# Performance work log

Hardware: AMD Instinct MI355X
Metric: run time of the kernel (lower is better)

## Reference

```python
import jax, jax.numpy as jnp
import numpy as np

EMBED_DIM = 1024
NUM_HEADS = 16
HEAD_DIM = EMBED_DIM // NUM_HEADS


def setup_inputs() -> dict:
    key = jax.random.key(0)
    k1, k2, k3, k4, k5 = jax.random.split(key, 5)
    B, T, C = 2, 2048, EMBED_DIM
    x = jax.random.normal(k1, (B, T, C), dtype=jnp.float32)
    # Linear params stored as (in, out) so y = x @ W + b
    s = 1.0 / np.sqrt(C)
    W_qkv = jax.random.uniform(k2, (C, 3 * C), minval=-s, maxval=s, dtype=jnp.float32)
    b_qkv = jax.random.uniform(k3, (3 * C,), minval=-s, maxval=s, dtype=jnp.float32)
    W_out = jax.random.uniform(k4, (C, C), minval=-s, maxval=s, dtype=jnp.float32)
    b_out = jax.random.uniform(k5, (C,), minval=-s, maxval=s, dtype=jnp.float32)
    return {"x": x, "W_qkv": W_qkv, "b_qkv": b_qkv, "W_out": W_out, "b_out": b_out}


def reference(x, W_qkv, b_qkv, W_out, b_out):
    B, T, C = x.shape
    H, D = NUM_HEADS, HEAD_DIM
    qkv = x @ W_qkv + b_qkv                       # [B, T, 3C]
    qkv = qkv.reshape(B, T, 3, H, D)
    q = qkv[:, :, 0].transpose(0, 2, 1, 3)        # [B, H, T, D]
    k = qkv[:, :, 1].transpose(0, 2, 1, 3)
    v = qkv[:, :, 2].transpose(0, 2, 1, 3)
    scores = jnp.einsum('bhqd,bhkd->bhqk', q, k) / jnp.sqrt(jnp.float32(D))
    causal = jnp.tril(jnp.ones((T, T), dtype=bool))
    scores = jnp.where(causal, scores, -jnp.inf)
    attn = jax.nn.softmax(scores, axis=-1)        # [B, H, T, T]
    out = jnp.einsum('bhqk,bhkd->bhqd', attn, v)  # [B, H, T, D]
    out = out.transpose(0, 2, 1, 3).reshape(B, T, C)
    out = out @ W_out + b_out
    return out
```

## Files before the change

kernel.cpp:

```cpp
#include <hip/hip_runtime.h>
#include <hip/hip_bf16.h>
#include <stdint.h>

typedef __bf16 bf16x8 __attribute__((ext_vector_type(8)));
typedef float  f32x4  __attribute__((ext_vector_type(4)));

typedef __attribute__((address_space(1))) void gas1_t;
typedef __attribute__((address_space(3))) void as3_t;

__device__ __forceinline__ void gload_lds16(const void* g, void* l) {
  __builtin_amdgcn_global_load_lds((gas1_t*)g, (as3_t*)l, 16, 0, 0);
}

__device__ __forceinline__ f32x4 zero4() { f32x4 z = {0.f, 0.f, 0.f, 0.f}; return z; }

__device__ __forceinline__ unsigned pack_bf16x2(float a, float b) {
  __bf16 ha = (__bf16)a, hb = (__bf16)b;
  unsigned short ua = *(unsigned short*)&ha, ub = *(unsigned short*)&hb;
  return (unsigned)ua | ((unsigned)ub << 16);
}

__global__ void cvt_f32_to_bf16(const float* __restrict__ in, __bf16* __restrict__ out, int n) {
  int i = (blockIdx.x * 256 + threadIdx.x) * 8;
  if (i >= n) return;
  const f32x4 v0 = *(const f32x4*)(in + i);
  const f32x4 v1 = *(const f32x4*)(in + i + 4);
  bf16x8 o;
#pragma unroll
  for (int j = 0; j < 4; ++j) { o[j] = (__bf16)v0[j]; o[j + 4] = (__bf16)v1[j]; }
  *(bf16x8*)(out + i) = o;
}

__global__ void transpose_cast(const float* __restrict__ W, __bf16* __restrict__ WT,
                               int K, int N) {
  __shared__ float tile[32][33];
  const int n0 = blockIdx.x * 32, k0 = blockIdx.y * 32;
  const int tx = threadIdx.x, ty = threadIdx.y;
  for (int i = ty; i < 32; i += 8) tile[i][tx] = W[(size_t)(k0 + i) * N + n0 + tx];
  __syncthreads();
  for (int i = ty; i < 32; i += 8) WT[(size_t)(n0 + i) * K + k0 + tx] = (__bf16)tile[tx][i];
}

template <int OUT_BF16, int A_F32, int SCALE_Q>
__global__ __launch_bounds__(256) void gemm_bt(const void* __restrict__ Ap,
                                               const __bf16* __restrict__ BT,
                                               const float* __restrict__ bias,
                                               void* __restrict__ Cout,
                                               int M, int N, int K) {
  __shared__ __bf16 As[2][4096];
  __shared__ __bf16 Bs[2][4096];
  const int tid = threadIdx.x;
  const int lane = tid & 63, w = tid >> 6;
  const int wr = w >> 1, wc = w & 1;
  const int lgrp = lane >> 4, lcol = lane & 15;
  const int m0 = blockIdx.y * 128, n0 = blockIdx.x * 128;

  f32x4 acc[4][4];
#pragma unroll
  for (int m = 0; m < 4; ++m)
#pragma unroll
    for (int n = 0; n < 4; ++n) acc[m][n] = zero4();

  const int nk = K >> 5;

  auto stageB = [&](int buf, int k0) {
#pragma unroll
    for (int q = 0; q < 2; ++q) {
      const int c = q * 256 + w * 64 + lane;
      const int row = c >> 2, kc = (c & 3) * 8;
      const int ldsoff = (q * 256 + w * 64) * 16;
      gload_lds16(BT + (size_t)(n0 + row) * K + k0 + kc, (char*)&Bs[buf][0] + ldsoff);
    }
  };
  auto stageA = [&](int buf, int k0) {
    if (A_F32) {
      const float* A = (const float*)Ap;
      const int c0 = tid * 2;
      const int row = c0 >> 2, kc = (c0 & 3) * 8;
      const float* src = A + (size_t)(m0 + row) * K + k0 + kc;
      const f32x4 v0 = *(const f32x4*)(src);
      const f32x4 v1 = *(const f32x4*)(src + 4);
      const f32x4 v2 = *(const f32x4*)(src + 8);
      const f32x4 v3 = *(const f32x4*)(src + 12);
      bf16x8 o0, o1;
#pragma unroll
      for (int j = 0; j < 4; ++j) {
        o0[j] = (__bf16)v0[j]; o0[j + 4] = (__bf16)v1[j];
        o1[j] = (__bf16)v2[j]; o1[j + 4] = (__bf16)v3[j];
      }
      *(bf16x8*)((char*)&As[buf][0] + c0 * 16) = o0;
      *(bf16x8*)((char*)&As[buf][0] + c0 * 16 + 16) = o1;
    } else {
      const __bf16* A = (const __bf16*)Ap;
#pragma unroll
      for (int q = 0; q < 2; ++q) {
        const int c = q * 256 + w * 64 + lane;
        const int row = c >> 2, kc = (c & 3) * 8;
        const int ldsoff = (q * 256 + w * 64) * 16;
        gload_lds16(A + (size_t)(m0 + row) * K + k0 + kc, (char*)&As[buf][0] + ldsoff);
      }
    }
  };

  stageA(0, 0);
  stageB(0, 0);
  __syncthreads();
  int cur = 0;
  for (int t = 0; t < nk; ++t) {
    if (t + 1 < nk) { stageA(cur ^ 1, (t + 1) * 32); stageB(cur ^ 1, (t + 1) * 32); }
    bf16x8 af[4], bfr[4];
#pragma unroll
    for (int m = 0; m < 4; ++m)
      af[m] = *(const bf16x8*)&As[cur][(wr * 64 + m * 16 + lcol) * 32 + lgrp * 8];
#pragma unroll
    for (int n = 0; n < 4; ++n)
      bfr[n] = *(const bf16x8*)&Bs[cur][(wc * 64 + n * 16 + lcol) * 32 + lgrp * 8];
    __builtin_amdgcn_s_setprio(1);
#pragma unroll
    for (int m = 0; m < 4; ++m)
#pragma unroll
      for (int n = 0; n < 4; ++n)
        acc[m][n] = __builtin_amdgcn_mfma_f32_16x16x32_bf16(af[m], bfr[n], acc[m][n], 0, 0, 0);
    __builtin_amdgcn_s_setprio(0);
    __syncthreads();
    cur ^= 1;
  }

#pragma unroll
  for (int m = 0; m < 4; ++m) {
#pragma unroll
    for (int n = 0; n < 4; ++n) {
      const int col = n0 + wc * 64 + n * 16 + lcol;
      const float bv = bias[col];
#pragma unroll
      for (int r = 0; r < 4; ++r) {
        const int row = m0 + wr * 64 + m * 16 + lgrp * 4 + r;
        float v = acc[m][n][r] + bv;
        if (SCALE_Q && col < 1024) v *= 0.125f;
        if (OUT_BF16)
          ((__bf16*)Cout)[(size_t)row * N + col] = (__bf16)v;
        else
          ((float*)Cout)[(size_t)row * N + col] = v;
      }
    }
  }
}

__global__ __launch_bounds__(512, 4) void attn_fused(const __bf16* __restrict__ qkv,
                                                     __bf16* __restrict__ attnb) {
  __shared__ __bf16 Kl[2][64][80];
  __shared__ __bf16 Vt[2][64][80];
  __shared__ __bf16 Pl[8][16][80];
  const int tid = threadIdx.x, lane = tid & 63, w = tid >> 6;
  const int lgrp = lane >> 4, lcol = lane & 15;
  const int bh = blockIdx.y;
  const int xp = (bh & 16) ? (15 - blockIdx.x) : blockIdx.x;
  const int b = bh >> 4, h = bh & 15;
  const __bf16* base = qkv + (size_t)b * 2048 * 3072;

  const int qb = xp * 128;
  const int rw = qb + w * 16;
  const int nkv = xp + 1;

  const int krow = tid >> 3;
  const int d00 = (tid & 7) * 8;
  const int vcol = ((((krow >> 3) ^ (tid & 7)) << 3) | (krow & 7));
  const __bf16* kvp = base + 1024 + h * 64 + d00;

  const int q_l = rw + lcol;
  const __bf16* qptr = base + (size_t)q_l * 3072 + h * 64;
  const bf16x8 qf0 = *(const bf16x8*)(qptr + lgrp * 8);
  const bf16x8 qf1 = *(const bf16x8*)(qptr + 32 + lgrp * 8);

  float m1 = -1e30f, l1 = 0.f;
  f32x4 acc_o[4];
#pragma unroll
  for (int d = 0; d < 4; ++d) acc_o[d] = zero4();

  bf16x8 kf0 = *(const bf16x8*)(kvp + (size_t)krow * 3072);
  bf16x8 vf0 = *(const bf16x8*)(kvp + (size_t)krow * 3072 + 1024);
  bf16x8 kf1 = *(const bf16x8*)(kvp + (size_t)(krow + 64) * 3072);
  bf16x8 vf1 = *(const bf16x8*)(kvp + (size_t)(krow + 64) * 3072 + 1024);

  for (int kvb = 0; kvb < nkv; ++kvb) {
    const int kv0 = kvb * 128;
    __syncthreads();
    *(bf16x8*)&Kl[0][krow][d00] = kf0;
    *(bf16x8*)&Kl[1][krow][d00] = kf1;
#pragma unroll
    for (int j = 0; j < 8; ++j) {
      Vt[0][d00 + j][vcol] = vf0[j];
      Vt[1][d00 + j][vcol] = vf1[j];
    }
    __syncthreads();
    if (kvb + 1 < nkv) {
      const __bf16* p = kvp + (size_t)(kv0 + 128 + krow) * 3072;
      kf0 = *(const bf16x8*)p;
      vf0 = *(const bf16x8*)(p + 1024);
      kf1 = *(const bf16x8*)(p + (size_t)64 * 3072);
      vf1 = *(const bf16x8*)(p + (size_t)64 * 3072 + 1024);
    }

    const bool diag = (kvb == xp);
    const bool skip1 = diag && (w < 4);

    f32x4 accs[8];
    __builtin_amdgcn_s_setprio(1);
#pragma unroll
    for (int sub = 0; sub < 4; ++sub) {
      accs[sub] = zero4();
#pragma unroll
      for (int s = 0; s < 2; ++s) {
        const bf16x8 kb = *(const bf16x8*)&Kl[0][sub * 16 + lcol][s * 32 + lgrp * 8];
        accs[sub] = __builtin_amdgcn_mfma_f32_16x16x32_bf16(kb, s ? qf1 : qf0, accs[sub], 0, 0, 0);
      }
    }
    if (!skip1) {
#pragma unroll
      for (int sub = 0; sub < 4; ++sub) {
        accs[4 + sub] = zero4();
#pragma unroll
        for (int s = 0; s < 2; ++s) {
          const bf16x8 kb = *(const bf16x8*)&Kl[1][sub * 16 + lcol][s * 32 + lgrp * 8];
          accs[4 + sub] = __builtin_amdgcn_mfma_f32_16x16x32_bf16(kb, s ? qf1 : qf0, accs[4 + sub], 0, 0, 0);
        }
      }
    } else {
#pragma unroll
      for (int sub = 4; sub < 8; ++sub) accs[sub] = f32x4{-1e30f, -1e30f, -1e30f, -1e30f};
    }
    __builtin_amdgcn_s_setprio(0);

    if (diag) {
#pragma unroll
      for (int sub = 0; sub < 8; ++sub) {
        const int kvg = kv0 + sub * 16 + lgrp * 4;
#pragma unroll
        for (int r = 0; r < 4; ++r)
          if (kvg + r > q_l) accs[sub][r] = -1e30f;
      }
    }

    float mx[8];
#pragma unroll
    for (int sub = 0; sub < 8; ++sub)
      mx[sub] = fmaxf(fmaxf(accs[sub][0], accs[sub][1]), fmaxf(accs[sub][2], accs[sub][3]));
    float rm = fmaxf(fmaxf(fmaxf(mx[0], mx[1]), fmaxf(mx[2], mx[3])),
                     fmaxf(fmaxf(mx[4], mx[5]), fmaxf(mx[6], mx[7])));
    rm = fmaxf(rm, __shfl_xor(rm, 16));
    rm = fmaxf(rm, __shfl_xor(rm, 32));
    const float nm = fmaxf(m1, rm);
    const float sf = __expf(m1 - nm);
    m1 = nm;

    float ps[8];
#pragma unroll
    for (int sub = 0; sub < 8; ++sub) {
#pragma unroll
      for (int r = 0; r < 4; ++r) accs[sub][r] = __expf(accs[sub][r] - nm);
      ps[sub] = (accs[sub][0] + accs[sub][1]) + (accs[sub][2] + accs[sub][3]);
    }
    float rs = ((ps[0] + ps[1]) + (ps[2] + ps[3])) + ((ps[4] + ps[5]) + (ps[6] + ps[7]));
    rs += __shfl_xor(rs, 16);
    rs += __shfl_xor(rs, 32);
    l1 = l1 * sf + rs;

#pragma unroll
    for (int d = 0; d < 4; ++d)
#pragma unroll
      for (int r = 0; r < 4; ++r) acc_o[d][r] *= sf;

#pragma unroll
    for (int sub = 0; sub < 4; ++sub) {
      uint2 pk;
      pk.x = pack_bf16x2(accs[sub][0], accs[sub][1]);
      pk.y = pack_bf16x2(accs[sub][2], accs[sub][3]);
      const int eoff = ((((sub * 2 + (lgrp >> 1)) ^ ((lcol >> 2) & 3)) << 3) | ((lgrp & 1) << 2));
      *(uint2*)&Pl[w][lcol][eoff] = pk;
    }
    asm volatile("s_waitcnt lgkmcnt(0)" ::: "memory");
    __builtin_amdgcn_sched_barrier(0);
    __builtin_amdgcn_s_setprio(1);
#pragma unroll
    for (int s = 0; s < 2; ++s) {
      const bf16x8 pf = *(const bf16x8*)&Pl[w][lcol][((4 * s + lgrp) ^ ((lcol >> 2) & 3)) * 8];
#pragma unroll
      for (int d = 0; d < 4; ++d) {
        const bf16x8 vfr = *(const bf16x8*)&Vt[0][d * 16 + lcol][((4 * s + lgrp) ^ ((2 * d + (lcol >> 3)) & 7)) * 8];
        acc_o[d] = __builtin_amdgcn_mfma_f32_16x16x32_bf16(vfr, pf, acc_o[d], 0, 0, 0);
      }
    }
    __builtin_amdgcn_s_setprio(0);

    if (!skip1) {
#pragma unroll
      for (int sub = 0; sub < 4; ++sub) {
        uint2 pk;
        pk.x = pack_bf16x2(accs[4 + sub][0], accs[4 + sub][1]);
        pk.y = pack_bf16x2(accs[4 + sub][2], accs[4 + sub][3]);
        const int eoff = ((((sub * 2 + (lgrp >> 1)) ^ ((lcol >> 2) & 3)) << 3) | ((lgrp & 1) << 2));
        *(uint2*)&Pl[w][lcol][eoff] = pk;
      }
      asm volatile("s_waitcnt lgkmcnt(0)" ::: "memory");
      __builtin_amdgcn_sched_barrier(0);
      __builtin_amdgcn_s_setprio(1);
#pragma unroll
      for (int s = 0; s < 2; ++s) {
        const bf16x8 pf = *(const bf16x8*)&Pl[w][lcol][((4 * s + lgrp) ^ ((lcol >> 2) & 3)) * 8];
#pragma unroll
        for (int d = 0; d < 4; ++d) {
          const bf16x8 vfr = *(const bf16x8*)&Vt[1][d * 16 + lcol][((4 * s + lgrp) ^ ((2 * d + (lcol >> 3)) & 7)) * 8];
          acc_o[d] = __builtin_amdgcn_mfma_f32_16x16x32_bf16(vfr, pf, acc_o[d], 0, 0, 0);
        }
      }
      __builtin_amdgcn_s_setprio(0);
    }
  }

  const float inv_l = 1.0f / l1;
  __bf16* orow = attnb + (size_t)(b * 2048 + q_l) * 1024 + h * 64 + lgrp * 4;
#pragma unroll
  for (int d = 0; d < 4; ++d) {
    uint2 ov;
    ov.x = pack_bf16x2(acc_o[d][0] * inv_l, acc_o[d][1] * inv_l);
    ov.y = pack_bf16x2(acc_o[d][2] * inv_l, acc_o[d][3] * inv_l);
    *(uint2*)(orow + d * 16) = ov;
  }
}

extern "C" void kernel_launch(void* const* d_in, const int* in_sizes, int n_in,
                              void* d_out, int out_size, void* d_ws, size_t ws_size,
                              hipStream_t stream) {
  const float* x    = (const float*)d_in[0];
  const float* Wqkv = (const float*)d_in[1];
  const float* bqkv = (const float*)d_in[2];
  const float* Wout = (const float*)d_in[3];
  const float* bout = (const float*)d_in[4];
  float* out = (float*)d_out;

  char* ws = (char*)d_ws;
  __bf16* qkvb  = (__bf16*)(ws);
  __bf16* wqkvT = (__bf16*)(ws + (24u << 20));
  __bf16* xb    = (__bf16*)(ws + (30u << 20));
  __bf16* attnb = (__bf16*)(ws + (24u << 20));
  __bf16* woutT = (__bf16*)(ws);

  const bool big_ws = ws_size >= ((size_t)38 << 20);

  transpose_cast<<<dim3(3072 / 32, 1024 / 32), dim3(32, 8), 0, stream>>>(Wqkv, wqkvT, 1024, 3072);

  if (big_ws) {
    cvt_f32_to_bf16<<<dim3(4096 * 1024 / 2048), dim3(256), 0, stream>>>(x, xb, 4096 * 1024);
    gemm_bt<1, 0, 1><<<dim3(3072 / 128, 4096 / 128), dim3(256), 0, stream>>>(
        (const void*)xb, wqkvT, bqkv, (void*)qkvb, 4096, 3072, 1024);
  } else {
    gemm_bt<1, 1, 1><<<dim3(3072 / 128, 4096 / 128), dim3(256), 0, stream>>>(
        (const void*)x, wqkvT, bqkv, (void*)qkvb, 4096, 3072, 1024);
  }

  attn_fused<<<dim3(16, 2 * 16), dim3(512), 0, stream>>>(qkvb, attnb);

  transpose_cast<<<dim3(1024 / 32, 1024 / 32), dim3(32, 8), 0, stream>>>(Wout, woutT, 1024, 1024);

  gemm_bt<0, 0, 0><<<dim3(1024 / 128, 4096 / 128), dim3(256), 0, stream>>>(
      (const void*)attnb, woutT, bout, (void*)out, 4096, 1024, 1024);
}
```

Baseline: 123.6 us.

## Give each attention wave two query groups and halve block size

```diff
diff --git a/kernel.cpp b/kernel.cpp
--- a/kernel.cpp
+++ b/kernel.cpp
@@ -146,185 +146,198 @@
   }
 }
 
-__global__ __launch_bounds__(512, 4) void attn_fused(const __bf16* __restrict__ qkv,
-                                                     __bf16* __restrict__ attnb) {
-  __shared__ __bf16 Kl[2][64][80];
-  __shared__ __bf16 Vt[2][64][80];
-  __shared__ __bf16 Pl[8][16][80];
+__global__ __launch_bounds__(256) void attn_fused(const __bf16* __restrict__ qkv,
+                                                  __bf16* __restrict__ attnb) {
+  __shared__ __bf16 Kl[2][64][64];
+  __shared__ __bf16 Vt[2][64][64];
+  __shared__ __bf16 Pl[4][2][16][64];
   const int tid = threadIdx.x, lane = tid & 63, w = tid >> 6;
   const int lgrp = lane >> 4, lcol = lane & 15;
   const int bh = blockIdx.y;
   const int xp = (bh & 16) ? (15 - blockIdx.x) : blockIdx.x;
-  const int b = bh >> 4, h = bh & 15;
+  const int b = bh >> 4, head = bh & 15;
   const __bf16* base = qkv + (size_t)b * 2048 * 3072;
 
   const int qb = xp * 128;
-  const int rw = qb + w * 16;
   const int nkv = xp + 1;
 
-  const int krow = tid >> 3;
-  const int d00 = (tid & 7) * 8;
-  const int vcol = ((((krow >> 3) ^ (tid & 7)) << 3) | (krow & 7));
-  const __bf16* kvp = base + 1024 + h * 64 + d00;
-
-  const int q_l = rw + lcol;
-  const __bf16* qptr = base + (size_t)q_l * 3072 + h * 64;
-  const bf16x8 qf0 = *(const bf16x8*)(qptr + lgrp * 8);
-  const bf16x8 qf1 = *(const bf16x8*)(qptr + 32 + lgrp * 8);
-
-  float m1 = -1e30f, l1 = 0.f;
-  f32x4 acc_o[4];
-#pragma unroll
-  for (int d = 0; d < 4; ++d) acc_o[d] = zero4();
-
-  bf16x8 kf0 = *(const bf16x8*)(kvp + (size_t)krow * 3072);
-  bf16x8 vf0 = *(const bf16x8*)(kvp + (size_t)krow * 3072 + 1024);
-  bf16x8 kf1 = *(const bf16x8*)(kvp + (size_t)(krow + 64) * 3072);
-  bf16x8 vf1 = *(const bf16x8*)(kvp + (size_t)(krow + 64) * 3072 + 1024);
+  const int krow = tid >> 2;
+  const int vpair = tid & 3;
+  const int kblk0 = (2 * vpair) ^ (krow & 7);
+  const int kblk1 = (2 * vpair + 1) ^ (krow & 7);
+  const int vblk0 = (krow >> 3) ^ (2 * vpair);
+  const int vblk1 = (krow >> 3) ^ (2 * vpair + 1);
+  const int velem = krow & 7;
+  const __bf16* kvp = base + 1024 + head * 64 + vpair * 16;
+
+  const int q_l0 = qb + w * 32 + lcol;
+  const int q_l1 = q_l0 + 16;
+  const __bf16* qp0 = base + (size_t)q_l0 * 3072 + head * 64 + lgrp * 8;
+  const __bf16* qp1 = base + (size_t)q_l1 * 3072 + head * 64 + lgrp * 8;
+  bf16x8 qf[2][2];
+  qf[0][0] = *(const bf16x8*)(qp0);      qf[0][1] = *(const bf16x8*)(qp0 + 32);
+  qf[1][0] = *(const bf16x8*)(qp1);      qf[1][1] = *(const bf16x8*)(qp1 + 32);
+
+  float m1[2] = {-1e30f, -1e30f}, l1[2] = {0.f, 0.f};
+  f32x4 acc_o[2][4];
+#pragma unroll
+  for (int qg = 0; qg < 2; ++qg)
+#pragma unroll
+    for (int d = 0; d < 4; ++d) acc_o[qg][d] = zero4();
+
+  bf16x8 kv_k[2][2], kv_v[2][2];
+#pragma unroll
+  for (int hf = 0; hf < 2; ++hf) {
+    const __bf16* p = kvp + (size_t)(hf * 64 + krow) * 3072;
+    kv_k[hf][0] = *(const bf16x8*)(p);
+    kv_k[hf][1] = *(const bf16x8*)(p + 8);
+    kv_v[hf][0] = *(const bf16x8*)(p + 1024);
+    kv_v[hf][1] = *(const bf16x8*)(p + 1032);
+  }
 
   for (int kvb = 0; kvb < nkv; ++kvb) {
     const int kv0 = kvb * 128;
     __syncthreads();
-    *(bf16x8*)&Kl[0][krow][d00] = kf0;
-    *(bf16x8*)&Kl[1][krow][d00] = kf1;
-#pragma unroll
-    for (int j = 0; j < 8; ++j) {
-      Vt[0][d00 + j][vcol] = vf0[j];
-      Vt[1][d00 + j][vcol] = vf1[j];
+#pragma unroll
+    for (int hf = 0; hf < 2; ++hf) {
+      *(bf16x8*)&Kl[hf][krow][kblk0 * 8] = kv_k[hf][0];
+      *(bf16x8*)&Kl[hf][krow][kblk1 * 8] = kv_k[hf][1];
+#pragma unroll
+      for (int j = 0; j < 8; ++j) {
+        Vt[hf][vpair * 16 + j][vblk0 * 8 + velem] = kv_v[hf][0][j];
+        Vt[hf][vpair * 16 + 8 + j][vblk1 * 8 + velem] = kv_v[hf][1][j];
+      }
     }
     __syncthreads();
     if (kvb + 1 < nkv) {
-      const __bf16* p = kvp + (size_t)(kv0 + 128 + krow) * 3072;
-      kf0 = *(const bf16x8*)p;
-      vf0 = *(const bf16x8*)(p + 1024);
-      kf1 = *(const bf16x8*)(p + (size_t)64 * 3072);
-      vf1 = *(const bf16x8*)(p + (size_t)64 * 3072 + 1024);
+#pragma unroll
+      for (int hf = 0; hf < 2; ++hf) {
+        const __bf16* p = kvp + (size_t)(kv0 + 128 + hf * 64 + krow) * 3072;
+        kv_k[hf][0] = *(const bf16x8*)(p);
+        kv_k[hf][1] = *(const bf16x8*)(p + 8);
+        kv_v[hf][0] = *(const bf16x8*)(p + 1024);
+        kv_v[hf][1] = *(const bf16x8*)(p + 1032);
+      }
     }
 
     const bool diag = (kvb == xp);
-    const bool skip1 = diag && (w < 4);
-
-    f32x4 accs[8];
+    const bool skip1 = diag && (w < 2);
+
+    f32x4 accs[2][8];
     __builtin_amdgcn_s_setprio(1);
 #pragma unroll
-    for (int sub = 0; sub < 4; ++sub) {
-      accs[sub] = zero4();
-#pragma unroll
-      for (int s = 0; s < 2; ++s) {
-        const bf16x8 kb = *(const bf16x8*)&Kl[0][sub * 16 + lcol][s * 32 + lgrp * 8];
-        accs[sub] = __builtin_amdgcn_mfma_f32_16x16x32_bf16(kb, s ? qf1 : qf0, accs[sub], 0, 0, 0);
-      }
-    }
-    if (!skip1) {
-#pragma unroll
-      for (int sub = 0; sub < 4; ++sub) {
-        accs[4 + sub] = zero4();
-#pragma unroll
-        for (int s = 0; s < 2; ++s) {
-          const bf16x8 kb = *(const bf16x8*)&Kl[1][sub * 16 + lcol][s * 32 + lgrp * 8];
-          accs[4 + sub] = __builtin_amdgcn_mfma_f32_16x16x32_bf16(kb, s ? qf1 : qf0, accs[4 + sub], 0, 0, 0);
+    for (int hf = 0; hf < 2; ++hf) {
+      if (hf == 1 && skip1) {
+#pragma unroll
+        for (int qg = 0; qg < 2; ++qg)
+#pragma unroll
+          for (int sub = 0; sub < 4; ++sub)
+            accs[qg][4 + sub] = f32x4{-1e30f, -1e30f, -1e30f, -1e30f};
+      } else {
+#pragma unroll
+        for (int sub = 0; sub < 4; ++sub) {
+          accs[0][hf * 4 + sub] = zero4();
+          accs[1][hf * 4 + sub] = zero4();
+#pragma unroll
+          for (int s = 0; s < 2; ++s) {
+            const bf16x8 kb = *(const bf16x8*)&Kl[hf][sub * 16 + lcol][((4 * s + lgrp) ^ (lcol & 7)) * 8];
+            accs[0][hf * 4 + sub] = __builtin_amdgcn_mfma_f32_16x16x32_bf16(kb, qf[0][s], accs[0][hf * 4 + sub], 0, 0, 0);
+            accs[1][hf * 4 + sub] = __builtin_amdgcn_mfma_f32_16x16x32_bf16(kb, qf[1][s], accs[1][hf * 4 + sub], 0, 0, 0);
+          }
         }
       }
-    } else {
-#pragma unroll
-      for (int sub = 4; sub < 8; ++sub) accs[sub] = f32x4{-1e30f, -1e30f, -1e30f, -1e30f};
     }
     __builtin_amdgcn_s_setprio(0);
 
     if (diag) {
-#pragma unroll
-      for (int sub = 0; sub < 8; ++sub) {
-        const int kvg = kv0 + sub * 16 + lgrp * 4;
-#pragma unroll
-        for (int r = 0; r < 4; ++r)
-          if (kvg + r > q_l) accs[sub][r] = -1e30f;
-      }
-    }
-
-    float mx[8];
-#pragma unroll
-    for (int sub = 0; sub < 8; ++sub)
-      mx[sub] = fmaxf(fmaxf(accs[sub][0], accs[sub][1]), fmaxf(accs[sub][2], accs[sub][3]));
-    float rm = fmaxf(fmaxf(fmaxf(mx[0], mx[1]), fmaxf(mx[2], mx[3])),
-                     fmaxf(fmaxf(mx[4], mx[5]), fmaxf(mx[6], mx[7])));
-    rm = fmaxf(rm, __shfl_xor(rm, 16));
-    rm = fmaxf(rm, __shfl_xor(rm, 32));
-    const float nm = fmaxf(m1, rm);
-    const float sf = __expf(m1 - nm);
-    m1 = nm;
-
-    float ps[8];
-#pragma unroll
-    for (int sub = 0; sub < 8; ++sub) {
-#pragma unroll
-      for (int r = 0; r < 4; ++r) accs[sub][r] = __expf(accs[sub][r] - nm);
-      ps[sub] = (accs[sub][0] + accs[sub][1]) + (accs[sub][2] + accs[sub][3]);
-    }
-    float rs = ((ps[0] + ps[1]) + (ps[2] + ps[3])) + ((ps[4] + ps[5]) + (ps[6] + ps[7]));
-    rs += __shfl_xor(rs, 16);
-    rs += __shfl_xor(rs, 32);
-    l1 = l1 * sf + rs;
-
-#pragma unroll
-    for (int d = 0; d < 4; ++d)
-#pragma unroll
-      for (int r = 0; r < 4; ++r) acc_o[d][r] *= sf;
-
-#pragma unroll
-    for (int sub = 0; sub < 4; ++sub) {
-      uint2 pk;
-      pk.x = pack_bf16x2(accs[sub][0], accs[sub][1]);
-      pk.y = pack_bf16x2(accs[sub][2], accs[sub][3]);
-      const int eoff = ((((sub * 2 + (lgrp >> 1)) ^ ((lcol >> 2) & 3)) << 3) | ((lgrp & 1) << 2));
-      *(uint2*)&Pl[w][lcol][eoff] = pk;
-    }
-    asm volatile("s_waitcnt lgkmcnt(0)" ::: "memory");
-    __builtin_amdgcn_sched_barrier(0);
-    __builtin_amdgcn_s_setprio(1);
-#pragma unroll
-    for (int s = 0; s < 2; ++s) {
-      const bf16x8 pf = *(const bf16x8*)&Pl[w][lcol][((4 * s + lgrp) ^ ((lcol >> 2) & 3)) * 8];
-#pragma unroll
-      for (int d = 0; d < 4; ++d) {
-        const bf16x8 vfr = *(const bf16x8*)&Vt[0][d * 16 + lcol][((4 * s + lgrp) ^ ((2 * d + (lcol >> 3)) & 7)) * 8];
-        acc_o[d] = __builtin_amdgcn_mfma_f32_16x16x32_bf16(vfr, pf, acc_o[d], 0, 0, 0);
-      }
-    }
-    __builtin_amdgcn_s_setprio(0);
-
-    if (!skip1) {
-#pragma unroll
-      for (int sub = 0; sub < 4; ++sub) {
-        uint2 pk;
-        pk.x = pack_bf16x2(accs[4 + sub][0], accs[4 + sub][1]);
-        pk.y = pack_bf16x2(accs[4 + sub][2], accs[4 + sub][3]);
-        const int eoff = ((((sub * 2 + (lgrp >> 1)) ^ ((lcol >> 2) & 3)) << 3) | ((lgrp & 1) << 2));
-        *(uint2*)&Pl[w][lcol][eoff] = pk;
+      const int qloc0 = w * 32 + lcol, qloc1 = qloc0 + 16;
+#pragma unroll
+      for (int i = 0; i < 8; ++i) {
+        const int kvl = (i >> 2) * 64 + (i & 3) * 16 + 4 * lgrp;
+#pragma unroll
+        for (int r = 0; r < 4; ++r) {
+          if (kvl + r > qloc0) accs[0][i][r] = -1e30f;
+          if (kvl + r > qloc1) accs[1][i][r] = -1e30f;
+        }
+      }
+    }
+
+    float sf[2];
+#pragma unroll
+    for (int qg = 0; qg < 2; ++qg) {
+      float mx[8];
+#pragma unroll
+      for (int i = 0; i < 8; ++i)
+        mx[i] = fmaxf(fmaxf(accs[qg][i][0], accs[qg][i][1]), fmaxf(accs[qg][i][2], accs[qg][i][3]));
+      float rm = fmaxf(fmaxf(fmaxf(mx[0], mx[1]), fmaxf(mx[2], mx[3])),
+                       fmaxf(fmaxf(mx[4], mx[5]), fmaxf(mx[6], mx[7])));
+      rm = fmaxf(rm, __shfl_xor(rm, 16));
+      rm = fmaxf(rm, __shfl_xor(rm, 32));
+      const float nm = fmaxf(m1[qg], rm);
+      sf[qg] = __expf(m1[qg] - nm);
+      m1[qg] = nm;
+      float ps[8];
+#pragma unroll
+      for (int i = 0; i < 8; ++i) {
+#pragma unroll
+        for (int r = 0; r < 4; ++r) accs[qg][i][r] = __expf(accs[qg][i][r] - nm);
+        ps[i] = (accs[qg][i][0] + accs[qg][i][1]) + (accs[qg][i][2] + accs[qg][i][3]);
+      }
+      float rs = ((ps[0] + ps[1]) + (ps[2] + ps[3])) + ((ps[4] + ps[5]) + (ps[6] + ps[7]));
+      rs += __shfl_xor(rs, 16);
+      rs += __shfl_xor(rs, 32);
+      l1[qg] = l1[qg] * sf[qg] + rs;
+#pragma unroll
+      for (int d = 0; d < 4; ++d)
+#pragma unroll
+        for (int r = 0; r < 4; ++r) acc_o[qg][d][r] *= sf[qg];
+    }
+
+#pragma unroll
+    for (int hf = 0; hf < 2; ++hf) {
+      if (hf == 1 && skip1) continue;
+#pragma unroll
+      for (int qg = 0; qg < 2; ++qg) {
+#pragma unroll
+        for (int sub = 0; sub < 4; ++sub) {
+          uint2 pk;
+          pk.x = pack_bf16x2(accs[qg][hf * 4 + sub][0], accs[qg][hf * 4 + sub][1]);
+          pk.y = pack_bf16x2(accs[qg][hf * 4 + sub][2], accs[qg][hf * 4 + sub][3]);
+          const int blk = (2 * sub + (lgrp >> 1)) ^ (lcol & 7);
+          *(uint2*)&Pl[w][qg][lcol][blk * 8 + (lgrp & 1) * 4] = pk;
+        }
       }
       asm volatile("s_waitcnt lgkmcnt(0)" ::: "memory");
       __builtin_amdgcn_sched_barrier(0);
       __builtin_amdgcn_s_setprio(1);
 #pragma unroll
       for (int s = 0; s < 2; ++s) {
-        const bf16x8 pf = *(const bf16x8*)&Pl[w][lcol][((4 * s + lgrp) ^ ((lcol >> 2) & 3)) * 8];
+        const int pblk = ((4 * s + lgrp) ^ (lcol & 7)) * 8;
+        const bf16x8 pf0 = *(const bf16x8*)&Pl[w][0][lcol][pblk];
+        const bf16x8 pf1 = *(const bf16x8*)&Pl[w][1][lcol][pblk];
 #pragma unroll
         for (int d = 0; d < 4; ++d) {
-          const bf16x8 vfr = *(const bf16x8*)&Vt[1][d * 16 + lcol][((4 * s + lgrp) ^ ((2 * d + (lcol >> 3)) & 7)) * 8];
-          acc_o[d] = __builtin_amdgcn_mfma_f32_16x16x32_bf16(vfr, pf, acc_o[d], 0, 0, 0);
+          const bf16x8 vfr = *(const bf16x8*)&Vt[hf][d * 16 + lcol][((4 * s + lgrp) ^ ((2 * d + (lcol >> 3)) & 7)) * 8];
+          acc_o[0][d] = __builtin_amdgcn_mfma_f32_16x16x32_bf16(vfr, pf0, acc_o[0][d], 0, 0, 0);
+          acc_o[1][d] = __builtin_amdgcn_mfma_f32_16x16x32_bf16(vfr, pf1, acc_o[1][d], 0, 0, 0);
         }
       }
       __builtin_amdgcn_s_setprio(0);
     }
   }
 
-  const float inv_l = 1.0f / l1;
-  __bf16* orow = attnb + (size_t)(b * 2048 + q_l) * 1024 + h * 64 + lgrp * 4;
-#pragma unroll
-  for (int d = 0; d < 4; ++d) {
-    uint2 ov;
-    ov.x = pack_bf16x2(acc_o[d][0] * inv_l, acc_o[d][1] * inv_l);
-    ov.y = pack_bf16x2(acc_o[d][2] * inv_l, acc_o[d][3] * inv_l);
-    *(uint2*)(orow + d * 16) = ov;
+#pragma unroll
+  for (int qg = 0; qg < 2; ++qg) {
+    const float inv_l = 1.0f / l1[qg];
+    const int q = (qg ? q_l1 : q_l0);
+    __bf16* orow = attnb + (size_t)(b * 2048 + q) * 1024 + head * 64 + lgrp * 4;
+#pragma unroll
+    for (int d = 0; d < 4; ++d) {
+      uint2 ov;
+      ov.x = pack_bf16x2(acc_o[qg][d][0] * inv_l, acc_o[qg][d][1] * inv_l);
+      ov.y = pack_bf16x2(acc_o[qg][d][2] * inv_l, acc_o[qg][d][3] * inv_l);
+      *(uint2*)(orow + d * 16) = ov;
+    }
   }
 }
 
@@ -358,7 +371,7 @@
         (const void*)x, wqkvT, bqkv, (void*)qkvb, 4096, 3072, 1024);
   }
 
-  attn_fused<<<dim3(16, 2 * 16), dim3(512), 0, stream>>>(qkvb, attnb);
+  attn_fused<<<dim3(16, 2 * 16), dim3(256), 0, stream>>>(qkvb, attnb);
 
   transpose_cast<<<dim3(1024 / 32, 1024 / 32), dim3(32, 8), 0, stream>>>(Wout, woutT, 1024, 1024);
 
```

Measured after the change: 158.2 us. 27.9% more time.

## Double-buffer K/V shared tiles with XOR swizzle in attention kernel

Applied to the files above, without the earlier changes.

```diff
diff --git a/kernel.cpp b/kernel.cpp
--- a/kernel.cpp
+++ b/kernel.cpp
@@ -146,29 +146,29 @@
   }
 }
 
-__global__ __launch_bounds__(512, 4) void attn_fused(const __bf16* __restrict__ qkv,
-                                                     __bf16* __restrict__ attnb) {
-  __shared__ __bf16 Kl[2][64][80];
-  __shared__ __bf16 Vt[2][64][80];
-  __shared__ __bf16 Pl[8][16][80];
+__global__ __launch_bounds__(512) void attn_fused(const __bf16* __restrict__ qkv,
+                                                  __bf16* __restrict__ attnb) {
+  __shared__ __bf16 Kl[2][2][64][64];
+  __shared__ __bf16 Vt[2][2][64][64];
+  __shared__ __bf16 Pl[8][16][64];
   const int tid = threadIdx.x, lane = tid & 63, w = tid >> 6;
   const int lgrp = lane >> 4, lcol = lane & 15;
   const int bh = blockIdx.y;
   const int xp = (bh & 16) ? (15 - blockIdx.x) : blockIdx.x;
-  const int b = bh >> 4, h = bh & 15;
+  const int b = bh >> 4, head = bh & 15;
   const __bf16* base = qkv + (size_t)b * 2048 * 3072;
 
   const int qb = xp * 128;
-  const int rw = qb + w * 16;
   const int nkv = xp + 1;
 
   const int krow = tid >> 3;
   const int d00 = (tid & 7) * 8;
+  const int kblk = ((tid & 7) ^ (krow & 7)) * 8;
   const int vcol = ((((krow >> 3) ^ (tid & 7)) << 3) | (krow & 7));
-  const __bf16* kvp = base + 1024 + h * 64 + d00;
-
-  const int q_l = rw + lcol;
-  const __bf16* qptr = base + (size_t)q_l * 3072 + h * 64;
+  const __bf16* kvp = base + 1024 + head * 64 + d00;
+
+  const int q_l = qb + w * 16 + lcol;
+  const __bf16* qptr = base + (size_t)q_l * 3072 + head * 64;
   const bf16x8 qf0 = *(const bf16x8*)(qptr + lgrp * 8);
   const bf16x8 qf1 = *(const bf16x8*)(qptr + 32 + lgrp * 8);
 
@@ -177,30 +177,34 @@
 #pragma unroll
   for (int d = 0; d < 4; ++d) acc_o[d] = zero4();
 
-  bf16x8 kf0 = *(const bf16x8*)(kvp + (size_t)krow * 3072);
-  bf16x8 vf0 = *(const bf16x8*)(kvp + (size_t)krow * 3072 + 1024);
-  bf16x8 kf1 = *(const bf16x8*)(kvp + (size_t)(krow + 64) * 3072);
-  bf16x8 vf1 = *(const bf16x8*)(kvp + (size_t)(krow + 64) * 3072 + 1024);
+  bf16x8 kf0, kf1, vf0, vf1;
+  auto load_tile = [&](int tau) {
+    const __bf16* p = kvp + (size_t)(tau * 128 + krow) * 3072;
+    kf0 = *(const bf16x8*)(p);
+    vf0 = *(const bf16x8*)(p + 1024);
+    kf1 = *(const bf16x8*)(p + (size_t)64 * 3072);
+    vf1 = *(const bf16x8*)(p + (size_t)64 * 3072 + 1024);
+  };
+  auto write_tile = [&](int buf) {
+    *(bf16x8*)&Kl[buf][0][krow][kblk] = kf0;
+    *(bf16x8*)&Kl[buf][1][krow][kblk] = kf1;
+#pragma unroll
+    for (int j = 0; j < 8; ++j) {
+      Vt[buf][0][d00 + j][vcol] = vf0[j];
+      Vt[buf][1][d00 + j][vcol] = vf1[j];
+    }
+  };
+
+  load_tile(0);
+  write_tile(0);
+  if (nkv > 1) load_tile(1);
 
   for (int kvb = 0; kvb < nkv; ++kvb) {
+    __syncthreads();
+    if (kvb + 1 < nkv) write_tile((kvb + 1) & 1);
+    if (kvb + 2 < nkv) load_tile(kvb + 2);
+    const int buf = kvb & 1;
     const int kv0 = kvb * 128;
-    __syncthreads();
-    *(bf16x8*)&Kl[0][krow][d00] = kf0;
-    *(bf16x8*)&Kl[1][krow][d00] = kf1;
-#pragma unroll
-    for (int j = 0; j < 8; ++j) {
-      Vt[0][d00 + j][vcol] = vf0[j];
-      Vt[1][d00 + j][vcol] = vf1[j];
-    }
-    __syncthreads();
-    if (kvb + 1 < nkv) {
-      const __bf16* p = kvp + (size_t)(kv0 + 128 + krow) * 3072;
-      kf0 = *(const bf16x8*)p;
-      vf0 = *(const bf16x8*)(p + 1024);
-      kf1 = *(const bf16x8*)(p + (size_t)64 * 3072);
-      vf1 = *(const bf16x8*)(p + (size_t)64 * 3072 + 1024);
-    }
-
     const bool diag = (kvb == xp);
     const bool skip1 = diag && (w < 4);
 
@@ -211,7 +215,7 @@
       accs[sub] = zero4();
 #pragma unroll
       for (int s = 0; s < 2; ++s) {
-        const bf16x8 kb = *(const bf16x8*)&Kl[0][sub * 16 + lcol][s * 32 + lgrp * 8];
+        const bf16x8 kb = *(const bf16x8*)&Kl[buf][0][sub * 16 + lcol][((4 * s + lgrp) ^ (lcol & 7)) * 8];
         accs[sub] = __builtin_amdgcn_mfma_f32_16x16x32_bf16(kb, s ? qf1 : qf0, accs[sub], 0, 0, 0);
       }
     }
@@ -221,7 +225,7 @@
         accs[4 + sub] = zero4();
 #pragma unroll
         for (int s = 0; s < 2; ++s) {
-          const bf16x8 kb = *(const bf16x8*)&Kl[1][sub * 16 + lcol][s * 32 + lgrp * 8];
+          const bf16x8 kb = *(const bf16x8*)&Kl[buf][1][sub * 16 + lcol][((4 * s + lgrp) ^ (lcol & 7)) * 8];
           accs[4 + sub] = __builtin_amdgcn_mfma_f32_16x16x32_bf16(kb, s ? qf1 : qf0, accs[4 + sub], 0, 0, 0);
         }
       }
@@ -271,45 +275,25 @@
       for (int r = 0; r < 4; ++r) acc_o[d][r] *= sf;
 
 #pragma unroll
-    for (int sub = 0; sub < 4; ++sub) {
-      uint2 pk;
-      pk.x = pack_bf16x2(accs[sub][0], accs[sub][1]);
-      pk.y = pack_bf16x2(accs[sub][2], accs[sub][3]);
-      const int eoff = ((((sub * 2 + (lgrp >> 1)) ^ ((lcol >> 2) & 3)) << 3) | ((lgrp & 1) << 2));
-      *(uint2*)&Pl[w][lcol][eoff] = pk;
-    }
-    asm volatile("s_waitcnt lgkmcnt(0)" ::: "memory");
-    __builtin_amdgcn_sched_barrier(0);
-    __builtin_amdgcn_s_setprio(1);
-#pragma unroll
-    for (int s = 0; s < 2; ++s) {
-      const bf16x8 pf = *(const bf16x8*)&Pl[w][lcol][((4 * s + lgrp) ^ ((lcol >> 2) & 3)) * 8];
-#pragma unroll
-      for (int d = 0; d < 4; ++d) {
-        const bf16x8 vfr = *(const bf16x8*)&Vt[0][d * 16 + lcol][((4 * s + lgrp) ^ ((2 * d + (lcol >> 3)) & 7)) * 8];
-        acc_o[d] = __builtin_amdgcn_mfma_f32_16x16x32_bf16(vfr, pf, acc_o[d], 0, 0, 0);
-      }
-    }
-    __builtin_amdgcn_s_setprio(0);
-
-    if (!skip1) {
+    for (int hf = 0; hf < 2; ++hf) {
+      if (hf == 1 && skip1) continue;
 #pragma unroll
       for (int sub = 0; sub < 4; ++sub) {
         uint2 pk;
-        pk.x = pack_bf16x2(accs[4 + sub][0], accs[4 + sub][1]);
-        pk.y = pack_bf16x2(accs[4 + sub][2], accs[4 + sub][3]);
-        const int eoff = ((((sub * 2 + (lgrp >> 1)) ^ ((lcol >> 2) & 3)) << 3) | ((lgrp & 1) << 2));
-        *(uint2*)&Pl[w][lcol][eoff] = pk;
+        pk.x = pack_bf16x2(accs[hf * 4 + sub][0], accs[hf * 4 + sub][1]);
+        pk.y = pack_bf16x2(accs[hf * 4 + sub][2], accs[hf * 4 + sub][3]);
+        const int blk = (2 * sub + (lgrp >> 1)) ^ (lcol & 7);
+        *(uint2*)&Pl[w][lcol][blk * 8 + (lgrp & 1) * 4] = pk;
       }
       asm volatile("s_waitcnt lgkmcnt(0)" ::: "memory");
       __builtin_amdgcn_sched_barrier(0);
       __builtin_amdgcn_s_setprio(1);
 #pragma unroll
       for (int s = 0; s < 2; ++s) {
-        const bf16x8 pf = *(const bf16x8*)&Pl[w][lcol][((4 * s + lgrp) ^ ((lcol >> 2) & 3)) * 8];
+        const bf16x8 pf = *(const bf16x8*)&Pl[w][lcol][((4 * s + lgrp) ^ (lcol & 7)) * 8];
 #pragma unroll
         for (int d = 0; d < 4; ++d) {
-          const bf16x8 vfr = *(const bf16x8*)&Vt[1][d * 16 + lcol][((4 * s + lgrp) ^ ((2 * d + (lcol >> 3)) & 7)) * 8];
+          const bf16x8 vfr = *(const bf16x8*)&Vt[buf][hf][d * 16 + lcol][((4 * s + lgrp) ^ ((2 * d + (lcol >> 3)) & 7)) * 8];
           acc_o[d] = __builtin_amdgcn_mfma_f32_16x16x32_bf16(vfr, pf, acc_o[d], 0, 0, 0);
         }
       }
@@ -318,7 +302,7 @@
   }
 
   const float inv_l = 1.0f / l1;
-  __bf16* orow = attnb + (size_t)(b * 2048 + q_l) * 1024 + h * 64 + lgrp * 4;
+  __bf16* orow = attnb + (size_t)(b * 2048 + q_l) * 1024 + head * 64 + lgrp * 4;
 #pragma unroll
   for (int d = 0; d < 4; ++d) {
     uint2 ov;
```

New measurement: 146.4 us. 1.18x slower.
